# Kernel optimization log

Measured on AMD Instinct MI355X. Metric: run time of the kernel, lower is better.

The kernel has to match this reference:

```python
import jax, jax.numpy as jnp
import numpy as np

B, T, IN_DIM, EMB = 8, 2048, 1024, 1024
NEG_INF = -1e30  # stand-in for float('-inf'); exp() underflows to 0 identically


def setup_inputs() -> dict:
    key = jax.random.key(0)
    ks = jax.random.split(key, 7)
    s = 1.0 / np.sqrt(IN_DIM)
    return {
        "x": jax.random.normal(ks[0], (B, T, IN_DIM), dtype=jnp.float32),
        "Wq": jax.random.normal(ks[1], (IN_DIM, EMB), dtype=jnp.float32) * s,
        "bq": jax.random.normal(ks[2], (EMB,), dtype=jnp.float32) * 0.01,
        "Wk": jax.random.normal(ks[3], (IN_DIM, EMB), dtype=jnp.float32) * s,
        "bk": jax.random.normal(ks[4], (EMB,), dtype=jnp.float32) * 0.01,
        "Wv": jax.random.normal(ks[5], (IN_DIM, EMB), dtype=jnp.float32) * s,
        "bv": jax.random.normal(ks[6], (EMB,), dtype=jnp.float32) * 0.01,
    }


def reference(x, Wq, bq, Wk, bk, Wv, bv):
    # projections: [B, T, EMB]
    q = x @ Wq + bq
    k = x @ Wk + bk
    v = x @ Wv + bv
    scale = jnp.asarray(EMB, x.dtype) ** 0.5
    # scores: [B, T, T]
    scores = jnp.einsum("btd,bsd->bts", q, k) / scale
    Tq = scores.shape[-2]
    causal = jnp.tril(jnp.ones((Tq, Tq), dtype=bool))  # [T, T]
    scores = jnp.where(causal, scores, jnp.asarray(NEG_INF, scores.dtype))
    # Faithful to torch.vmap(softmax): per-batch GLOBAL-matrix softmax
    # (max and sum taken over the whole [T, T] matrix, not per row).
    m = jnp.max(scores, axis=(-2, -1), keepdims=True)
    e = jnp.exp(scores - m)
    w = e / jnp.sum(e, axis=(-2, -1), keepdims=True)
    # output: [B, T, EMB]
    return jnp.einsum("bts,bsd->btd", w, v)
```

## Files before the change

### kernel.cpp

```cpp
#include <hip/hip_runtime.h>
#include <stdint.h>


#define B_   8
#define T_   2048
#define DIM  1024

typedef _Float16 f16;
typedef f16   f16x8 __attribute__((ext_vector_type(8)));
typedef f16   f16x4 __attribute__((ext_vector_type(4)));
typedef float f32x4 __attribute__((ext_vector_type(4)));

typedef const __attribute__((address_space(1))) void gvoid_t;
typedef __attribute__((address_space(3))) void lvoid_t;

__device__ __forceinline__ void stage_half256(const uint16_t* __restrict__ g, int ld,
                                              uint16_t* s, int tid) {
#pragma unroll
  for (int j = 0; j < 2; ++j) {
    int r   = j * 64 + (tid >> 3);
    int seg = (tid & 7) ^ (r & 7);
    const uint16_t* gp = g + (size_t)r * ld + seg * 8;
    uint16_t* sp = s + j * 4096 + (tid >> 6) * 512;
    __builtin_amdgcn_global_load_lds((gvoid_t*)gp, (lvoid_t*)sp, 16, 0, 0);
  }
}

__device__ __forceinline__ f16x8 frag64(const uint16_t* s, int r, int gseg) {
  return *(const f16x8*)(s + r * 64 + ((gseg ^ (r & 7)) * 8));
}

__device__ __forceinline__ void stage_u8k(const uint16_t* __restrict__ g, int ld,
                                          uint16_t* s, int tid) {
  int r   = tid >> 2;
  int seg = (tid & 3) ^ ((r >> 1) & 3);
  const uint16_t* gp = g + (size_t)r * ld + seg * 8;
  uint16_t* sp = s + (tid >> 6) * 512;
  __builtin_amdgcn_global_load_lds((gvoid_t*)gp, (lvoid_t*)sp, 16, 0, 0);
}

__device__ __forceinline__ f16x8 frag32(const uint16_t* s, int r, int gseg) {
  return *(const f16x8*)(s + r * 32 + ((gseg ^ ((r >> 1) & 3)) * 8));
}

__device__ __forceinline__ void lda4(const uint16_t* s, int rbase, int quad, int l15,
                                     f16x8 o[4][2]) {
#pragma unroll
  for (int mf = 0; mf < 4; ++mf) {
    int r = rbase + mf * 16 + l15;
#pragma unroll
    for (int kk = 0; kk < 2; ++kk) o[mf][kk] = frag64(s, r, kk * 4 + quad);
  }
}

__device__ __forceinline__ void ldb1(const uint16_t* s, int rbase, int quad, int l15,
                                     f16x8 o[2]) {
  int r = rbase + l15;
#pragma unroll
  for (int kk = 0; kk < 2; ++kk) o[kk] = frag64(s, r, kk * 4 + quad);
}

template <int M0, int N0>
__device__ __forceinline__ void mm8(f16x8 a[4][2], f16x8 b[2], f32x4 (&acc)[8][2]) {
#pragma unroll
  for (int kk = 0; kk < 2; ++kk)
#pragma unroll
    for (int mf = 0; mf < 4; ++mf)
      acc[M0 + mf][N0] = __builtin_amdgcn_mfma_f32_16x16x32_f16(
          a[mf][kk], b[kk], acc[M0 + mf][N0], 0, 0, 0);
}

#define SYNC_MFMA8(AA, BB, M0, N0)                     \
  __builtin_amdgcn_s_barrier();                        \
  asm volatile("s_waitcnt lgkmcnt(0)" ::: "memory");   \
  __builtin_amdgcn_s_setprio(1);                       \
  mm8<M0, N0>(AA, BB, acc);                            \
  __builtin_amdgcn_s_setprio(0);                       \
  __builtin_amdgcn_s_barrier();

__device__ __forceinline__ void gemm256_1bar(const uint16_t* __restrict__ gA,
                                             const uint16_t* __restrict__ gB,
                                             int lda, int ldb, int nTiles,
                                             uint16_t* smem, f32x4 (&acc)[8][4]) {
  const int tid = threadIdx.x, lane = tid & 63;
  const int quad = lane >> 4, l15 = lane & 15;
  const int wv = tid >> 6, wr = wv >> 2, wc = wv & 3;

#define STAGE_T(tt)                                                      \
  { uint16_t* sa = smem + ((tt) % 3) * 8192;                             \
    uint16_t* sb = smem + 24576 + ((tt) % 3) * 8192;                     \
    const uint16_t* ga = gA + (tt) * 32;                                 \
    const uint16_t* gb = gB + (tt) * 32;                                 \
    stage_u8k(ga,                     lda, sa,        tid);              \
    stage_u8k(ga + 128 * (size_t)lda, lda, sa + 4096, tid);              \
    stage_u8k(gb,                     ldb, sb,        tid);              \
    stage_u8k(gb + 128 * (size_t)ldb, ldb, sb + 4096, tid); }

#define READS_T(tt)                                                      \
  { const uint16_t* sa = smem + ((tt) % 3) * 8192;                       \
    const uint16_t* sb = smem + 24576 + ((tt) % 3) * 8192;               \
    _Pragma("unroll")                                                    \
    for (int mf = 0; mf < 8; ++mf)                                       \
      a[mf] = frag32(sa, wr * 128 + mf * 16 + l15, quad);                \
    _Pragma("unroll")                                                    \
    for (int nf = 0; nf < 4; ++nf)                                       \
      b[nf] = frag32(sb, wc * 64 + nf * 16 + l15, quad); }

#define MFMA_T                                                           \
  __builtin_amdgcn_s_setprio(1);                                         \
  _Pragma("unroll")                                                      \
  for (int mf = 0; mf < 8; ++mf)                                         \
    _Pragma("unroll")                                                    \
    for (int nf = 0; nf < 4; ++nf)                                       \
      acc[mf][nf] = __builtin_amdgcn_mfma_f32_16x16x32_f16(              \
          a[mf], b[nf], acc[mf][nf], 0, 0, 0);                           \
  __builtin_amdgcn_s_setprio(0);

  STAGE_T(0)
  STAGE_T(1)
  asm volatile("s_waitcnt vmcnt(4)" ::: "memory");
  __builtin_amdgcn_s_barrier();

  f16x8 a[8], b[4];
#pragma unroll 1
  for (int t = 0; t < nTiles - 2; ++t) {
    STAGE_T(t + 2)
    READS_T(t)
    MFMA_T
    __builtin_amdgcn_s_barrier();
    asm volatile("s_waitcnt vmcnt(4)" ::: "memory");
  }
  READS_T(nTiles - 2)
  MFMA_T
  __builtin_amdgcn_s_barrier();
  asm volatile("s_waitcnt vmcnt(0)" ::: "memory");
  READS_T(nTiles - 1)
  MFMA_T
#undef STAGE_T
#undef READS_T
#undef MFMA_T
}

__device__ __forceinline__ void gemm256n128_8ph(const uint16_t* __restrict__ gA,
                                                const uint16_t* __restrict__ gB,
                                                int lda, int ldb, int nIter,
                                                uint16_t* smem, f32x4 (&acc)[8][2]) {
  const int tid = threadIdx.x, lane = tid & 63;
  const int quad = lane >> 4, l15 = lane & 15;
  const int wv = tid >> 6, wr = wv >> 2, wc = wv & 3;

  uint16_t* sA0 = smem;
  uint16_t* sA1 = smem + 16384;
  uint16_t* sB0 = smem + 32768;
  uint16_t* sB1 = smem + 40960;

  stage_half256(gA,                     lda, sA0,        tid);
  stage_half256(gA + 128 * (size_t)lda, lda, sA0 + 8192, tid);
  stage_half256(gB,                     ldb, sB0,        tid);
  stage_half256(gB + 64,                ldb, sB1,        tid);
  asm volatile("s_waitcnt vmcnt(2)" ::: "memory");
  __builtin_amdgcn_s_barrier();

  f16x8 alo[4][2], ahi[4][2], b0[2], b1[2];
#pragma unroll 1
  for (int it = 0; it < nIter - 1; ++it) {
    const int t1 = 2 * it + 1, t2 = 2 * it + 2, t3 = 2 * it + 3;
    const uint16_t* gA1 = gA + t1 * 64;
    const uint16_t* gA2 = gA + t2 * 64;

    lda4(sA0, wr * 128,      quad, l15, alo);
    ldb1(sB0, wc * 32,       quad, l15, b0);
    stage_half256(gA1, lda, sA1, tid);
    SYNC_MFMA8(alo, b0, 0, 0)
    ldb1(sB0, wc * 32 + 16,  quad, l15, b1);
    stage_half256(gA1 + 128 * (size_t)lda, lda, sA1 + 8192, tid);
    SYNC_MFMA8(alo, b1, 0, 1)
    lda4(sA0, wr * 128 + 64, quad, l15, ahi);
    stage_half256(gB + t2 * 64, ldb, sB0, tid);
    SYNC_MFMA8(ahi, b1, 4, 1)
    asm volatile("s_waitcnt vmcnt(2)" ::: "memory");
    SYNC_MFMA8(ahi, b0, 4, 0)
    lda4(sA1, wr * 128,      quad, l15, alo);
    ldb1(sB1, wc * 32,       quad, l15, b0);
    stage_half256(gA2, lda, sA0, tid);
    SYNC_MFMA8(alo, b0, 0, 0)
    ldb1(sB1, wc * 32 + 16,  quad, l15, b1);
    stage_half256(gA2 + 128 * (size_t)lda, lda, sA0 + 8192, tid);
    SYNC_MFMA8(alo, b1, 0, 1)
    lda4(sA1, wr * 128 + 64, quad, l15, ahi);
    stage_half256(gB + t3 * 64, ldb, sB1, tid);
    SYNC_MFMA8(ahi, b1, 4, 1)
    asm volatile("s_waitcnt vmcnt(2)" ::: "memory");
    SYNC_MFMA8(ahi, b0, 4, 0)
  }
  {
    const uint16_t* gA1 = gA + (2 * nIter - 1) * 64;
    lda4(sA0, wr * 128,      quad, l15, alo);
    ldb1(sB0, wc * 32,       quad, l15, b0);
    stage_half256(gA1, lda, sA1, tid);
    SYNC_MFMA8(alo, b0, 0, 0)
    ldb1(sB0, wc * 32 + 16,  quad, l15, b1);
    stage_half256(gA1 + 128 * (size_t)lda, lda, sA1 + 8192, tid);
    SYNC_MFMA8(alo, b1, 0, 1)
    lda4(sA0, wr * 128 + 64, quad, l15, ahi);
    SYNC_MFMA8(ahi, b1, 4, 1)
    asm volatile("s_waitcnt vmcnt(0)" ::: "memory");
    SYNC_MFMA8(ahi, b0, 4, 0)
    lda4(sA1, wr * 128,      quad, l15, alo);
    ldb1(sB1, wc * 32,       quad, l15, b0);
    SYNC_MFMA8(alo, b0, 0, 0)
    ldb1(sB1, wc * 32 + 16,  quad, l15, b1);
    SYNC_MFMA8(alo, b1, 0, 1)
    lda4(sA1, wr * 128 + 64, quad, l15, ahi);
    SYNC_MFMA8(ahi, b1, 4, 1)
    SYNC_MFMA8(ahi, b0, 4, 0)
  }
}

__device__ __forceinline__ void zero_acc8(f32x4 (&acc)[8][4]) {
  f32x4 z = {0.f, 0.f, 0.f, 0.f};
#pragma unroll
  for (int i = 0; i < 8; ++i)
#pragma unroll
    for (int j = 0; j < 4; ++j) acc[i][j] = z;
}


__global__ void zero_lrow_kernel(float* __restrict__ lrow) {
  lrow[blockIdx.x * 256 + threadIdx.x] = 0.f;
}

__global__ void conv_x_kernel(const float* __restrict__ x, f16* __restrict__ xf) {
  size_t i = (size_t)blockIdx.x * 256 + threadIdx.x;
  float4 v = ((const float4*)x)[i];
  f16x4 o = {(f16)v.x, (f16)v.y, (f16)v.z, (f16)v.w};
  ((f16x4*)xf)[i] = o;
}

__global__ void convT_w_kernel(const float* __restrict__ Wq, const float* __restrict__ Wk,
                               const float* __restrict__ Wv, f16* __restrict__ WT) {
  __shared__ float tile[64][65];
  const int z = blockIdx.z;
  const float* W = (z == 0) ? Wq : (z == 1) ? Wk : Wv;
  const int r0 = blockIdx.x * 64, c0 = blockIdx.y * 64, tid = threadIdx.x;
#pragma unroll
  for (int i = 0; i < 16; ++i) {
    int rr = (tid >> 6) + 4 * i, cc = tid & 63;
    tile[rr][cc] = W[(size_t)(r0 + rr) * DIM + c0 + cc];
  }
  __syncthreads();
#pragma unroll
  for (int i = 0; i < 16; ++i) {
    int nn = (tid >> 6) + 4 * i, kk = tid & 63;
    WT[(size_t)z * DIM * DIM + (size_t)(c0 + nn) * DIM + r0 + kk] = (f16)tile[kk][nn];
  }
}

__global__ void reduce_z_kernel(const float* __restrict__ lrow, float* __restrict__ invZ) {
  const int b = blockIdx.x, tid = threadIdx.x;
  float s = 0.f;
  for (int i = tid; i < T_; i += 256) s += lrow[(size_t)b * T_ + i];
#pragma unroll
  for (int off = 1; off < 64; off <<= 1) s += __shfl_xor(s, off, 64);
  __shared__ float red[4];
  if ((tid & 63) == 0) red[tid >> 6] = s;
  __syncthreads();
  if (tid == 0) invZ[b] = 1.0f / (red[0] + red[1] + red[2] + red[3]);
}


__global__ __launch_bounds__(512, 2) void proj_kernel(
    const f16* __restrict__ xf, const f16* __restrict__ WT,
    const float* __restrict__ bq, const float* __restrict__ bk, const float* __restrict__ bv,
    f16* __restrict__ q, f16* __restrict__ k, f16* __restrict__ vT) {
  __shared__ uint16_t smem[49152];

  const int bid = blockIdx.x;
  const int xcd = bid & 7, local = bid >> 3;
  const int bx = xcd * 8 + (local & 7);
  const int zy = local >> 3;
  const int z = zy >> 2, by = zy & 3;
  const size_t arow = (size_t)bx * 256;
  const int    bcol = by * 256;

  f32x4 acc[8][4];
  zero_acc8(acc);
  gemm256_1bar((const uint16_t*)xf + arow * DIM,
               (const uint16_t*)WT + (size_t)z * DIM * DIM + (size_t)bcol * DIM,
               DIM, DIM, 32, smem, acc);

  const float* bias = (z == 0) ? bq : (z == 1) ? bk : bv;
  const int tid = threadIdx.x, lane = tid & 63, wv = tid >> 6;
  const int quad = lane >> 4, l15 = lane & 15;
  const int wr = wv >> 2, wc = wv & 3;
  if (z < 2) {
    f16* O = z ? k : q;
#pragma unroll
    for (int mf = 0; mf < 8; ++mf)
#pragma unroll
      for (int nf = 0; nf < 4; ++nf) {
        int n = bcol + wc * 64 + nf * 16 + l15;
        float bb = bias[n];
        size_t row0 = arow + wr * 128 + mf * 16 + quad * 4;
#pragma unroll
        for (int r = 0; r < 4; ++r)
          O[(row0 + r) * DIM + n] = (f16)(acc[mf][nf][r] + bb);
      }
  } else {
#pragma unroll
    for (int mf = 0; mf < 8; ++mf)
#pragma unroll
      for (int nf = 0; nf < 4; ++nf) {
        int n = bcol + wc * 64 + nf * 16 + l15;
        float bb = bias[n];
        int row0 = (int)arow + wr * 128 + mf * 16 + quad * 4;
        int bb_i = row0 >> 11, t0 = row0 & 2047;
        f16x4 pk;
#pragma unroll
        for (int r = 0; r < 4; ++r) pk[r] = (f16)(acc[mf][nf][r] + bb);
        *(f16x4*)(vT + ((size_t)bb_i * DIM + n) * T_ + t0) = pk;
      }
  }
}

__global__ __launch_bounds__(512, 2) void scores_kernel(
    const f16* __restrict__ q, const f16* __restrict__ k,
    f16* __restrict__ E, float* __restrict__ lrow) {
  __shared__ uint16_t smem[49152];
  const int bid = blockIdx.x;
  const int b = bid & 7, tri = bid >> 3;
  int qi = 0;
  while ((qi + 1) * (qi + 2) / 2 <= tri) ++qi;
  const int ki = tri - qi * (qi + 1) / 2;

  f32x4 acc[8][4];
  zero_acc8(acc);
  gemm256_1bar((const uint16_t*)(q + ((size_t)b * T_ + qi * 256) * DIM),
               (const uint16_t*)(k + ((size_t)b * T_ + ki * 256) * DIM),
               DIM, DIM, 32, smem, acc);

  const int tid = threadIdx.x, lane = tid & 63, wv = tid >> 6;
  const int quad = lane >> 4, l15 = lane & 15;
  const int wr = wv >> 2, wc = wv & 3;
  f16*   Eb = E + (size_t)b * T_ * T_;
  float* lb = lrow + (size_t)b * T_;
  const bool diag = (ki == qi);
#pragma unroll
  for (int mf = 0; mf < 8; ++mf) {
    float rs[4] = {0.f, 0.f, 0.f, 0.f};
#pragma unroll
    for (int nf = 0; nf < 4; ++nf)
#pragma unroll
      for (int r = 0; r < 4; ++r) {
        int t = qi * 256 + wr * 128 + mf * 16 + quad * 4 + r;
        int s = ki * 256 + wc * 64 + nf * 16 + l15;
        float e = 0.f;
        if (!diag || s <= t) e = __expf(fminf(acc[mf][nf][r] * 0.03125f, 11.f));
        Eb[(size_t)t * T_ + s] = (f16)e;
        rs[r] += e;
      }
#pragma unroll
    for (int off = 1; off < 16; off <<= 1)
#pragma unroll
      for (int r = 0; r < 4; ++r) rs[r] += __shfl_xor(rs[r], off, 64);
    if (l15 == 0)
#pragma unroll
      for (int r = 0; r < 4; ++r)
        atomicAdd(&lb[qi * 256 + wr * 128 + mf * 16 + quad * 4 + r], rs[r]);
  }
}

__global__ __launch_bounds__(512, 2) void pv_kernel(
    const f16* __restrict__ E, const f16* __restrict__ vT,
    const float* __restrict__ invZ, float* __restrict__ out) {
  __shared__ uint16_t smem[49152];
  const int bid = blockIdx.x;
  const int b = bid & 7, local = bid >> 3;
  const int nt = local & 7, pair = local >> 3;

  const float iz = invZ[b];
  const int tid = threadIdx.x, lane = tid & 63, wv = tid >> 6;
  const int quad = lane >> 4, l15 = lane & 15;
  const int wr = wv >> 2, wc = wv & 3;
  float* ob = out + (size_t)b * T_ * DIM;
  const uint16_t* Bv = (const uint16_t*)(vT + ((size_t)b * DIM + nt * 128) * (size_t)T_);

#pragma unroll 1
  for (int j = 0; j < 2; ++j) {
    const int qi = j ? (7 - pair) : pair;
    f32x4 acc[8][2];
    {
      f32x4 z = {0.f, 0.f, 0.f, 0.f};
#pragma unroll
      for (int i = 0; i < 8; ++i) { acc[i][0] = z; acc[i][1] = z; }
    }
    gemm256n128_8ph((const uint16_t*)(E + ((size_t)b * T_ + qi * 256) * (size_t)T_),
                    Bv, T_, T_, (qi + 1) * 2, smem, acc);
#pragma unroll
    for (int mf = 0; mf < 8; ++mf)
#pragma unroll
      for (int nf = 0; nf < 2; ++nf)
#pragma unroll
        for (int r = 0; r < 4; ++r) {
          int t = qi * 256 + wr * 128 + mf * 16 + quad * 4 + r;
          int n = nt * 128 + wc * 32 + nf * 16 + l15;
          ob[(size_t)t * DIM + n] = acc[mf][nf][r] * iz;
        }
  }
}


extern "C" void kernel_launch(void* const* d_in, const int* in_sizes, int n_in,
                              void* d_out, int out_size, void* d_ws, size_t ws_size,
                              hipStream_t stream) {
  const float* x  = (const float*)d_in[0];
  const float* Wq = (const float*)d_in[1];
  const float* bq = (const float*)d_in[2];
  const float* Wk = (const float*)d_in[3];
  const float* bk = (const float*)d_in[4];
  const float* Wv = (const float*)d_in[5];
  const float* bv = (const float*)d_in[6];
  float* out = (float*)d_out;

  char* ws = (char*)d_ws;
  f16*   E    = (f16*)ws;
  f16*   xf   = (f16*)ws;
  f16*   q    = (f16*)(ws + 67108864);
  f16*   k    = (f16*)(ws + 100663296);
  f16*   vT   = (f16*)(ws + 134217728);
  f16*   WT   = (f16*)(ws + 167772160);
  float* lrow = (float*)(ws + 174063616);
  float* invZ = (float*)(ws + 174129152);
  if (ws_size < (size_t)174129184) return;

  zero_lrow_kernel<<<64, 256, 0, stream>>>(lrow);
  conv_x_kernel<<<16384, 256, 0, stream>>>(x, xf);
  convT_w_kernel<<<dim3(16, 16, 3), 256, 0, stream>>>(Wq, Wk, Wv, WT);
  proj_kernel<<<dim3(768), 512, 0, stream>>>(xf, WT, bq, bk, bv, q, k, vT);
  scores_kernel<<<dim3(288), 512, 0, stream>>>(q, k, E, lrow);
  reduce_z_kernel<<<B_, 256, 0, stream>>>(lrow, invZ);
  pv_kernel<<<dim3(256), 512, 0, stream>>>(E, vT, invZ, out);
}
```

Measured before the change: 354.1 us.

## Double-buffer A fragments to overlap LDS reads with MFMA in 256x256 GEMM

Restructures the 3-stage LDS GEMM main loop into a 2x unrolled loop with two register sets for A fragments, so the next tile's A fragments are read from LDS while the current tile's MFMAs run. The global-load wait moves from vmcnt(4) placed after the barrier to vmcnt(0) placed before it, and the tail is rewritten to match. This aims to hide LDS read latency behind matrix ops. In exchange it adds 8 more f16x8 registers per thread, which may hurt occupancy at 2 blocks per CU, and it waits on the newest prefetch earlier than before.

```diff
diff --git a/kernel.cpp b/kernel.cpp
--- a/kernel.cpp
+++ b/kernel.cpp
@@ -78,10 +78,10 @@
   __builtin_amdgcn_s_setprio(0);                       \
   __builtin_amdgcn_s_barrier();
 
-__device__ __forceinline__ void gemm256_1bar(const uint16_t* __restrict__ gA,
-                                             const uint16_t* __restrict__ gB,
-                                             int lda, int ldb, int nTiles,
-                                             uint16_t* smem, f32x4 (&acc)[8][4]) {
+__device__ __forceinline__ void gemm256_ovl(const uint16_t* __restrict__ gA,
+                                            const uint16_t* __restrict__ gB,
+                                            int lda, int ldb, int nTiles,
+                                            uint16_t* smem, f32x4 (&acc)[8][4]) {
   const int tid = threadIdx.x, lane = tid & 63;
   const int quad = lane >> 4, l15 = lane & 15;
   const int wv = tid >> 6, wr = wv >> 2, wc = wv & 3;
@@ -96,48 +96,59 @@
     stage_u8k(gb,                     ldb, sb,        tid);              \
     stage_u8k(gb + 128 * (size_t)ldb, ldb, sb + 4096, tid); }
 
-#define READS_T(tt)                                                      \
+#define RA_T(tt, AV)                                                     \
   { const uint16_t* sa = smem + ((tt) % 3) * 8192;                       \
-    const uint16_t* sb = smem + 24576 + ((tt) % 3) * 8192;               \
     _Pragma("unroll")                                                    \
     for (int mf = 0; mf < 8; ++mf)                                       \
-      a[mf] = frag32(sa, wr * 128 + mf * 16 + l15, quad);                \
+      AV[mf] = frag32(sa, wr * 128 + mf * 16 + l15, quad); }
+
+#define RB_T(tt)                                                         \
+  { const uint16_t* sb = smem + 24576 + ((tt) % 3) * 8192;               \
     _Pragma("unroll")                                                    \
     for (int nf = 0; nf < 4; ++nf)                                       \
       b[nf] = frag32(sb, wc * 64 + nf * 16 + l15, quad); }
 
-#define MFMA_T                                                           \
+#define MFMA_T(AV)                                                       \
   __builtin_amdgcn_s_setprio(1);                                         \
   _Pragma("unroll")                                                      \
   for (int mf = 0; mf < 8; ++mf)                                         \
     _Pragma("unroll")                                                    \
     for (int nf = 0; nf < 4; ++nf)                                       \
       acc[mf][nf] = __builtin_amdgcn_mfma_f32_16x16x32_f16(              \
-          a[mf], b[nf], acc[mf][nf], 0, 0, 0);                           \
+          AV[mf], b[nf], acc[mf][nf], 0, 0, 0);                          \
   __builtin_amdgcn_s_setprio(0);
 
   STAGE_T(0)
   STAGE_T(1)
-  asm volatile("s_waitcnt vmcnt(4)" ::: "memory");
+  asm volatile("s_waitcnt vmcnt(0)" ::: "memory");
   __builtin_amdgcn_s_barrier();
 
-  f16x8 a[8], b[4];
+  f16x8 a0[8], a1[8], b[4];
+  RA_T(0, a0)
 #pragma unroll 1
-  for (int t = 0; t < nTiles - 2; ++t) {
+  for (int it = 0; it < nTiles / 2 - 1; ++it) {
+    const int t = 2 * it;
     STAGE_T(t + 2)
-    READS_T(t)
-    MFMA_T
+    RB_T(t)
+    RA_T(t + 1, a1)
+    MFMA_T(a0)
+    asm volatile("s_waitcnt vmcnt(0)" ::: "memory");
     __builtin_amdgcn_s_barrier();
-    asm volatile("s_waitcnt vmcnt(4)" ::: "memory");
-  }
-  READS_T(nTiles - 2)
-  MFMA_T
-  __builtin_amdgcn_s_barrier();
-  asm volatile("s_waitcnt vmcnt(0)" ::: "memory");
-  READS_T(nTiles - 1)
-  MFMA_T
+    STAGE_T(t + 3)
+    RB_T(t + 1)
+    RA_T(t + 2, a0)
+    MFMA_T(a1)
+    asm volatile("s_waitcnt vmcnt(0)" ::: "memory");
+    __builtin_amdgcn_s_barrier();
+  }
+  RB_T(nTiles - 2)
+  RA_T(nTiles - 1, a1)
+  MFMA_T(a0)
+  RB_T(nTiles - 1)
+  MFMA_T(a1)
 #undef STAGE_T
-#undef READS_T
+#undef RA_T
+#undef RB_T
 #undef MFMA_T
 }
 
@@ -285,9 +296,9 @@
 
   f32x4 acc[8][4];
   zero_acc8(acc);
-  gemm256_1bar((const uint16_t*)xf + arow * DIM,
-               (const uint16_t*)WT + (size_t)z * DIM * DIM + (size_t)bcol * DIM,
-               DIM, DIM, 32, smem, acc);
+  gemm256_ovl((const uint16_t*)xf + arow * DIM,
+              (const uint16_t*)WT + (size_t)z * DIM * DIM + (size_t)bcol * DIM,
+              DIM, DIM, 32, smem, acc);
 
   const float* bias = (z == 0) ? bq : (z == 1) ? bk : bv;
   const int tid = threadIdx.x, lane = tid & 63, wv = tid >> 6;
@@ -335,9 +346,9 @@
 
   f32x4 acc[8][4];
   zero_acc8(acc);
-  gemm256_1bar((const uint16_t*)(q + ((size_t)b * T_ + qi * 256) * DIM),
-               (const uint16_t*)(k + ((size_t)b * T_ + ki * 256) * DIM),
-               DIM, DIM, 32, smem, acc);
+  gemm256_ovl((const uint16_t*)(q + ((size_t)b * T_ + qi * 256) * DIM),
+              (const uint16_t*)(k + ((size_t)b * T_ + ki * 256) * DIM),
+              DIM, DIM, 32, smem, acc);
 
   const int tid = threadIdx.x, lane = tid & 63, wv = tid >> 6;
   const int quad = lane >> 4, l15 = lane & 15;
```

Result: no change. 358.4 us (+1.2%).

## Switch QK and projection GEMMs to 4-wave 32x32 MFMA tiles

Applied to the files above, without the earlier changes.

Rewrites the shared 256x256 GEMM to use 4 waves of 128x128 tiles with 32x32x16 MFMA instructions and ping-pong register fragments, staging more rows per thread. This raises arithmetic intensity per LDS read and reduces instruction issue overhead for the projection and scores kernels. It lowers occupancy to one 256-thread block and greatly increases accumulator register pressure, and epilogue indexing and row-sum reductions are reworked for the 32x32 output layout.

```diff
diff --git a/kernel.cpp b/kernel.cpp
--- a/kernel.cpp
+++ b/kernel.cpp
@@ -10,6 +10,7 @@
 typedef f16   f16x8 __attribute__((ext_vector_type(8)));
 typedef f16   f16x4 __attribute__((ext_vector_type(4)));
 typedef float f32x4 __attribute__((ext_vector_type(4)));
+typedef float f32x16 __attribute__((ext_vector_type(16)));
 
 typedef const __attribute__((address_space(1))) void gvoid_t;
 typedef __attribute__((address_space(3))) void lvoid_t;
@@ -30,17 +31,20 @@
   return *(const f16x8*)(s + r * 64 + ((gseg ^ (r & 7)) * 8));
 }
 
-__device__ __forceinline__ void stage_u8k(const uint16_t* __restrict__ g, int ld,
-                                          uint16_t* s, int tid) {
-  int r   = tid >> 2;
-  int seg = (tid & 3) ^ ((r >> 1) & 3);
-  const uint16_t* gp = g + (size_t)r * ld + seg * 8;
-  uint16_t* sp = s + (tid >> 6) * 512;
-  __builtin_amdgcn_global_load_lds((gvoid_t*)gp, (lvoid_t*)sp, 16, 0, 0);
-}
-
 __device__ __forceinline__ f16x8 frag32(const uint16_t* s, int r, int gseg) {
   return *(const f16x8*)(s + r * 32 + ((gseg ^ ((r >> 1) & 3)) * 8));
+}
+
+__device__ __forceinline__ void stage_t32(const uint16_t* __restrict__ g, int ld,
+                                          uint16_t* s, int tid) {
+#pragma unroll
+  for (int j = 0; j < 4; ++j) {
+    int r   = j * 64 + (tid >> 2);
+    int seg = (tid & 3) ^ ((r >> 1) & 3);
+    const uint16_t* gp = g + (size_t)r * ld + seg * 8;
+    uint16_t* sp = s + j * 2048 + (tid >> 6) * 512;
+    __builtin_amdgcn_global_load_lds((gvoid_t*)gp, (lvoid_t*)sp, 16, 0, 0);
+  }
 }
 
 __device__ __forceinline__ void lda4(const uint16_t* s, int rbase, int quad, int l15,
@@ -78,67 +82,72 @@
   __builtin_amdgcn_s_setprio(0);                       \
   __builtin_amdgcn_s_barrier();
 
-__device__ __forceinline__ void gemm256_1bar(const uint16_t* __restrict__ gA,
-                                             const uint16_t* __restrict__ gB,
-                                             int lda, int ldb, int nTiles,
-                                             uint16_t* smem, f32x4 (&acc)[8][4]) {
+__device__ __forceinline__ void gemm256_w32(const uint16_t* __restrict__ gA,
+                                            const uint16_t* __restrict__ gB,
+                                            int lda, int ldb, int nT,
+                                            uint16_t* smem, f32x16 (&acc)[4][4]) {
   const int tid = threadIdx.x, lane = tid & 63;
-  const int quad = lane >> 4, l15 = lane & 15;
-  const int wv = tid >> 6, wr = wv >> 2, wc = wv & 3;
-
-#define STAGE_T(tt)                                                      \
-  { uint16_t* sa = smem + ((tt) % 3) * 8192;                             \
-    uint16_t* sb = smem + 24576 + ((tt) % 3) * 8192;                     \
-    const uint16_t* ga = gA + (tt) * 32;                                 \
-    const uint16_t* gb = gB + (tt) * 32;                                 \
-    stage_u8k(ga,                     lda, sa,        tid);              \
-    stage_u8k(ga + 128 * (size_t)lda, lda, sa + 4096, tid);              \
-    stage_u8k(gb,                     ldb, sb,        tid);              \
-    stage_u8k(gb + 128 * (size_t)ldb, ldb, sb + 4096, tid); }
-
-#define READS_T(tt)                                                      \
+  const int l31 = lane & 31, half = lane >> 5;
+  const int wv = tid >> 6, wr = wv >> 1, wc = wv & 1;
+
+#define STG(tt)                                                          \
+  { stage_t32(gA + (tt) * 32, lda, smem + ((tt) % 3) * 8192, tid);       \
+    stage_t32(gB + (tt) * 32, ldb, smem + 24576 + ((tt) % 3) * 8192, tid); }
+
+#define RD(tt, AV, BV)                                                   \
   { const uint16_t* sa = smem + ((tt) % 3) * 8192;                       \
     const uint16_t* sb = smem + 24576 + ((tt) % 3) * 8192;               \
     _Pragma("unroll")                                                    \
-    for (int mf = 0; mf < 8; ++mf)                                       \
-      a[mf] = frag32(sa, wr * 128 + mf * 16 + l15, quad);                \
+    for (int ks = 0; ks < 2; ++ks) {                                     \
+      _Pragma("unroll")                                                  \
+      for (int mt = 0; mt < 4; ++mt)                                     \
+        AV[ks][mt] = frag32(sa, wr * 128 + mt * 32 + l31, ks * 2 + half);\
+      _Pragma("unroll")                                                  \
+      for (int nt = 0; nt < 4; ++nt)                                     \
+        BV[ks][nt] = frag32(sb, wc * 128 + nt * 32 + l31, ks * 2 + half);\
+    } }
+
+#define MM(AV, BV)                                                       \
+  { __builtin_amdgcn_s_setprio(1);                                       \
     _Pragma("unroll")                                                    \
-    for (int nf = 0; nf < 4; ++nf)                                       \
-      b[nf] = frag32(sb, wc * 64 + nf * 16 + l15, quad); }
-
-#define MFMA_T                                                           \
-  __builtin_amdgcn_s_setprio(1);                                         \
-  _Pragma("unroll")                                                      \
-  for (int mf = 0; mf < 8; ++mf)                                         \
-    _Pragma("unroll")                                                    \
-    for (int nf = 0; nf < 4; ++nf)                                       \
-      acc[mf][nf] = __builtin_amdgcn_mfma_f32_16x16x32_f16(              \
-          a[mf], b[nf], acc[mf][nf], 0, 0, 0);                           \
-  __builtin_amdgcn_s_setprio(0);
-
-  STAGE_T(0)
-  STAGE_T(1)
-  asm volatile("s_waitcnt vmcnt(4)" ::: "memory");
+    for (int ks = 0; ks < 2; ++ks)                                       \
+      _Pragma("unroll")                                                  \
+      for (int mt = 0; mt < 4; ++mt)                                     \
+        _Pragma("unroll")                                                \
+        for (int nt = 0; nt < 4; ++nt)                                   \
+          acc[mt][nt] = __builtin_amdgcn_mfma_f32_32x32x16_f16(          \
+              AV[ks][mt], BV[ks][nt], acc[mt][nt], 0, 0, 0);             \
+    __builtin_amdgcn_s_setprio(0); }
+
+  STG(0)
+  STG(1)
+  asm volatile("s_waitcnt vmcnt(8)" ::: "memory");
   __builtin_amdgcn_s_barrier();
 
-  f16x8 a[8], b[4];
+  f16x8 aA[2][4], bA[2][4], aB[2][4], bB[2][4];
+  RD(0, aA, bA)
 #pragma unroll 1
-  for (int t = 0; t < nTiles - 2; ++t) {
-    STAGE_T(t + 2)
-    READS_T(t)
-    MFMA_T
+  for (int it = 0; it < (nT - 2) / 2; ++it) {
+    const int t = 2 * it;
+    STG(t + 2)
+    asm volatile("s_waitcnt vmcnt(8)" ::: "memory");
     __builtin_amdgcn_s_barrier();
-    asm volatile("s_waitcnt vmcnt(4)" ::: "memory");
-  }
-  READS_T(nTiles - 2)
-  MFMA_T
+    RD(t + 1, aB, bB)
+    MM(aA, bA)
+    STG(t + 3)
+    asm volatile("s_waitcnt vmcnt(8)" ::: "memory");
+    __builtin_amdgcn_s_barrier();
+    RD(t + 2, aA, bA)
+    MM(aB, bB)
+  }
+  asm volatile("s_waitcnt vmcnt(0)" ::: "memory");
   __builtin_amdgcn_s_barrier();
-  asm volatile("s_waitcnt vmcnt(0)" ::: "memory");
-  READS_T(nTiles - 1)
-  MFMA_T
-#undef STAGE_T
-#undef READS_T
-#undef MFMA_T
+  RD(nT - 1, aB, bB)
+  MM(aA, bA)
+  MM(aB, bB)
+#undef STG
+#undef RD
+#undef MM
 }
 
 __device__ __forceinline__ void gemm256n128_8ph(const uint16_t* __restrict__ gA,
@@ -217,14 +226,6 @@
   }
 }
 
-__device__ __forceinline__ void zero_acc8(f32x4 (&acc)[8][4]) {
-  f32x4 z = {0.f, 0.f, 0.f, 0.f};
-#pragma unroll
-  for (int i = 0; i < 8; ++i)
-#pragma unroll
-    for (int j = 0; j < 4; ++j) acc[i][j] = z;
-}
-
 
 __global__ void zero_lrow_kernel(float* __restrict__ lrow) {
   lrow[blockIdx.x * 256 + threadIdx.x] = 0.f;
@@ -269,7 +270,7 @@
 }
 
 
-__global__ __launch_bounds__(512, 2) void proj_kernel(
+__global__ __launch_bounds__(256, 1) void proj_kernel(
     const f16* __restrict__ xf, const f16* __restrict__ WT,
     const float* __restrict__ bq, const float* __restrict__ bk, const float* __restrict__ bv,
     f16* __restrict__ q, f16* __restrict__ k, f16* __restrict__ vT) {
@@ -283,47 +284,55 @@
   const size_t arow = (size_t)bx * 256;
   const int    bcol = by * 256;
 
-  f32x4 acc[8][4];
-  zero_acc8(acc);
-  gemm256_1bar((const uint16_t*)xf + arow * DIM,
-               (const uint16_t*)WT + (size_t)z * DIM * DIM + (size_t)bcol * DIM,
-               DIM, DIM, 32, smem, acc);
+  f32x16 acc[4][4];
+#pragma unroll
+  for (int i = 0; i < 4; ++i)
+#pragma unroll
+    for (int j = 0; j < 4; ++j) acc[i][j] = (f32x16)(0.f);
+
+  gemm256_w32((const uint16_t*)xf + arow * DIM,
+              (const uint16_t*)WT + (size_t)z * DIM * DIM + (size_t)bcol * DIM,
+              DIM, DIM, 32, smem, acc);
 
   const float* bias = (z == 0) ? bq : (z == 1) ? bk : bv;
-  const int tid = threadIdx.x, lane = tid & 63, wv = tid >> 6;
-  const int quad = lane >> 4, l15 = lane & 15;
-  const int wr = wv >> 2, wc = wv & 3;
+  const int tid = threadIdx.x, lane = tid & 63;
+  const int l31 = lane & 31, half = lane >> 5;
+  const int wv = tid >> 6, wr = wv >> 1, wc = wv & 1;
   if (z < 2) {
     f16* O = z ? k : q;
 #pragma unroll
-    for (int mf = 0; mf < 8; ++mf)
-#pragma unroll
-      for (int nf = 0; nf < 4; ++nf) {
-        int n = bcol + wc * 64 + nf * 16 + l15;
+    for (int mt = 0; mt < 4; ++mt)
+#pragma unroll
+      for (int nt = 0; nt < 4; ++nt) {
+        int n = bcol + wc * 128 + nt * 32 + l31;
         float bb = bias[n];
-        size_t row0 = arow + wr * 128 + mf * 16 + quad * 4;
-#pragma unroll
-        for (int r = 0; r < 4; ++r)
-          O[(row0 + r) * DIM + n] = (f16)(acc[mf][nf][r] + bb);
+#pragma unroll
+        for (int g = 0; g < 16; ++g) {
+          size_t row = arow + wr * 128 + mt * 32 + (g & 3) + 8 * (g >> 2) + 4 * half;
+          O[row * DIM + n] = (f16)(acc[mt][nt][g] + bb);
+        }
       }
   } else {
 #pragma unroll
-    for (int mf = 0; mf < 8; ++mf)
-#pragma unroll
-      for (int nf = 0; nf < 4; ++nf) {
-        int n = bcol + wc * 64 + nf * 16 + l15;
+    for (int mt = 0; mt < 4; ++mt)
+#pragma unroll
+      for (int nt = 0; nt < 4; ++nt) {
+        int n = bcol + wc * 128 + nt * 32 + l31;
         float bb = bias[n];
-        int row0 = (int)arow + wr * 128 + mf * 16 + quad * 4;
-        int bb_i = row0 >> 11, t0 = row0 & 2047;
-        f16x4 pk;
-#pragma unroll
-        for (int r = 0; r < 4; ++r) pk[r] = (f16)(acc[mf][nf][r] + bb);
-        *(f16x4*)(vT + ((size_t)bb_i * DIM + n) * T_ + t0) = pk;
+#pragma unroll
+        for (int r4 = 0; r4 < 4; ++r4) {
+          int row0 = (int)arow + wr * 128 + mt * 32 + 8 * r4 + 4 * half;
+          int bb_i = row0 >> 11, t0 = row0 & 2047;
+          f16x4 pk;
+#pragma unroll
+          for (int rl = 0; rl < 4; ++rl) pk[rl] = (f16)(acc[mt][nt][r4 * 4 + rl] + bb);
+          *(f16x4*)(vT + ((size_t)bb_i * DIM + n) * T_ + t0) = pk;
+        }
       }
   }
 }
 
-__global__ __launch_bounds__(512, 2) void scores_kernel(
+__global__ __launch_bounds__(256, 1) void scores_kernel(
     const f16* __restrict__ q, const f16* __restrict__ k,
     f16* __restrict__ E, float* __restrict__ lrow) {
   __shared__ uint16_t smem[49152];
@@ -333,40 +342,47 @@
   while ((qi + 1) * (qi + 2) / 2 <= tri) ++qi;
   const int ki = tri - qi * (qi + 1) / 2;
 
-  f32x4 acc[8][4];
-  zero_acc8(acc);
-  gemm256_1bar((const uint16_t*)(q + ((size_t)b * T_ + qi * 256) * DIM),
-               (const uint16_t*)(k + ((size_t)b * T_ + ki * 256) * DIM),
-               DIM, DIM, 32, smem, acc);
-
-  const int tid = threadIdx.x, lane = tid & 63, wv = tid >> 6;
-  const int quad = lane >> 4, l15 = lane & 15;
-  const int wr = wv >> 2, wc = wv & 3;
+  f32x16 acc[4][4];
+#pragma unroll
+  for (int i = 0; i < 4; ++i)
+#pragma unroll
+    for (int j = 0; j < 4; ++j) acc[i][j] = (f32x16)(0.f);
+
+  gemm256_w32((const uint16_t*)(q + ((size_t)b * T_ + qi * 256) * DIM),
+              (const uint16_t*)(k + ((size_t)b * T_ + ki * 256) * DIM),
+              DIM, DIM, 32, smem, acc);
+
+  const int tid = threadIdx.x, lane = tid & 63;
+  const int l31 = lane & 31, half = lane >> 5;
+  const int wv = tid >> 6, wr = wv >> 1, wc = wv & 1;
   f16*   Eb = E + (size_t)b * T_ * T_;
   float* lb = lrow + (size_t)b * T_;
   const bool diag = (ki == qi);
 #pragma unroll
-  for (int mf = 0; mf < 8; ++mf) {
-    float rs[4] = {0.f, 0.f, 0.f, 0.f};
-#pragma unroll
-    for (int nf = 0; nf < 4; ++nf)
-#pragma unroll
-      for (int r = 0; r < 4; ++r) {
-        int t = qi * 256 + wr * 128 + mf * 16 + quad * 4 + r;
-        int s = ki * 256 + wc * 64 + nf * 16 + l15;
+  for (int mt = 0; mt < 4; ++mt) {
+    float rs[16];
+#pragma unroll
+    for (int g = 0; g < 16; ++g) rs[g] = 0.f;
+#pragma unroll
+    for (int nt = 0; nt < 4; ++nt)
+#pragma unroll
+      for (int g = 0; g < 16; ++g) {
+        int t = qi * 256 + wr * 128 + mt * 32 + (g & 3) + 8 * (g >> 2) + 4 * half;
+        int s = ki * 256 + wc * 128 + nt * 32 + l31;
         float e = 0.f;
-        if (!diag || s <= t) e = __expf(fminf(acc[mf][nf][r] * 0.03125f, 11.f));
+        if (!diag || s <= t) e = __expf(fminf(acc[mt][nt][g] * 0.03125f, 11.f));
         Eb[(size_t)t * T_ + s] = (f16)e;
-        rs[r] += e;
+        rs[g] += e;
       }
 #pragma unroll
-    for (int off = 1; off < 16; off <<= 1)
-#pragma unroll
-      for (int r = 0; r < 4; ++r) rs[r] += __shfl_xor(rs[r], off, 64);
-    if (l15 == 0)
-#pragma unroll
-      for (int r = 0; r < 4; ++r)
-        atomicAdd(&lb[qi * 256 + wr * 128 + mf * 16 + quad * 4 + r], rs[r]);
+    for (int off = 1; off < 32; off <<= 1)
+#pragma unroll
+      for (int g = 0; g < 16; ++g) rs[g] += __shfl_xor(rs[g], off, 64);
+    if (l31 == 0)
+#pragma unroll
+      for (int g = 0; g < 16; ++g)
+        atomicAdd(&lb[qi * 256 + wr * 128 + mt * 32 + (g & 3) + 8 * (g >> 2) + 4 * half],
+                  rs[g]);
   }
 }
 
@@ -436,8 +452,8 @@
   zero_lrow_kernel<<<64, 256, 0, stream>>>(lrow);
   conv_x_kernel<<<16384, 256, 0, stream>>>(x, xf);
   convT_w_kernel<<<dim3(16, 16, 3), 256, 0, stream>>>(Wq, Wk, Wv, WT);
-  proj_kernel<<<dim3(768), 512, 0, stream>>>(xf, WT, bq, bk, bv, q, k, vT);
-  scores_kernel<<<dim3(288), 512, 0, stream>>>(q, k, E, lrow);
+  proj_kernel<<<dim3(768), 256, 0, stream>>>(xf, WT, bq, bk, bv, q, k, vT);
+  scores_kernel<<<dim3(288), 256, 0, stream>>>(q, k, E, lrow);
   reduce_z_kernel<<<B_, 256, 0, stream>>>(lrow, invZ);
   pv_kernel<<<dim3(256), 512, 0, stream>>>(E, vT, invZ, out);
 }
```

Result: slower. 394.2 us (+11.3%).
